# Optimization experiments

Hardware: AMD Instinct MI355X
Metric: run time of the kernel (lower is better)

Reference implementation:

```python
import jax, jax.numpy as jnp
import numpy as np

B, T, I, H = 256, 512, 3, 32  # batch, seq_len, input_size, hidden_size


def setup_inputs() -> dict:
    key = jax.random.key(0)
    ks = jax.random.split(key, 24)
    bound = 1.0 / np.sqrt(H)  # PyTorch LSTM init: U(-1/sqrt(H), 1/sqrt(H))

    def u(k, shape):
        return jax.random.uniform(k, shape, jnp.float32, -bound, bound)

    inp = {"x": jax.random.normal(ks[0], (B, T, I), jnp.float32)}
    idx = 1
    for l, insz in [(0, I), (1, 2 * H)]:
        for d in "fb":
            inp[f"w_ih_l{l}{d}"] = u(ks[idx], (4 * H, insz)); idx += 1
            inp[f"w_hh_l{l}{d}"] = u(ks[idx], (4 * H, H)); idx += 1
            inp[f"b_ih_l{l}{d}"] = u(ks[idx], (4 * H,)); idx += 1
            inp[f"b_hh_l{l}{d}"] = u(ks[idx], (4 * H,)); idx += 1
    inp["wc1"] = u(ks[idx], (32, 2 * H)); idx += 1
    inp["bc1"] = u(ks[idx], (32,)); idx += 1
    inp["wc2"] = u(ks[idx], (2, 32)); idx += 1
    inp["bc2"] = u(ks[idx], (2,))
    return inp


def _lstm_dir(x, w_ih, w_hh, b_ih, b_hh, reverse):
    """One direction of one LSTM layer. x: [B,T,in]. Returns (hs [B,T,H], h_final [B,H])."""
    Bb, Hh = x.shape[0], w_hh.shape[1]
    # precompute input contribution for all timesteps: [T,B,4H]
    gx = jnp.einsum('bti,gi->tbg', x, w_ih) + (b_ih + b_hh)

    def step(carry, g):
        h, c = carry
        z = g + h @ w_hh.T  # [B,4H], gate order i,f,g,o (PyTorch)
        i, f, gg, o = jnp.split(z, 4, axis=-1)
        c = jax.nn.sigmoid(f) * c + jax.nn.sigmoid(i) * jnp.tanh(gg)
        h = jax.nn.sigmoid(o) * jnp.tanh(c)
        return (h, c), h

    init = (jnp.zeros((Bb, Hh), x.dtype), jnp.zeros((Bb, Hh), x.dtype))
    (h_final, _), hs = jax.lax.scan(step, init, gx, reverse=reverse)
    return jnp.swapaxes(hs, 0, 1), h_final


def reference(x,
              w_ih_l0f, w_hh_l0f, b_ih_l0f, b_hh_l0f,
              w_ih_l0b, w_hh_l0b, b_ih_l0b, b_hh_l0b,
              w_ih_l1f, w_hh_l1f, b_ih_l1f, b_hh_l1f,
              w_ih_l1b, w_hh_l1b, b_ih_l1b, b_hh_l1b,
              wc1, bc1, wc2, bc2):
    # Layer 0, both directions (dropout between layers disabled: eval mode)
    hs0f, _ = _lstm_dir(x, w_ih_l0f, w_hh_l0f, b_ih_l0f, b_hh_l0f, False)
    hs0b, _ = _lstm_dir(x, w_ih_l0b, w_hh_l0b, b_ih_l0b, b_hh_l0b, True)
    h0 = jnp.concatenate([hs0f, hs0b], axis=-1)  # [B,T,2H]
    # Layer 1: only final hidden states needed
    _, h1f = _lstm_dir(h0, w_ih_l1f, w_hh_l1f, b_ih_l1f, b_hh_l1f, False)
    _, h1b = _lstm_dir(h0, w_ih_l1b, w_hh_l1b, b_ih_l1b, b_hh_l1b, True)
    hn = jnp.concatenate([h1f, h1b], axis=-1)  # [B,2H] == torch.cat([hn[-2], hn[-1]], 1)
    # Classifier head (Dropout is identity in eval)
    hidden = jax.nn.relu(hn @ wc1.T + bc1)
    return hidden @ wc2.T + bc2  # [B,2] logits
```

## Files before the change

### kernel.cpp

```cpp
#include <hip/hip_runtime.h>
#include <cstdint>

#define T_SEQ 512
#define BATCH 256
#define HID   32

__device__ __forceinline__ float rcp_fast(float x) {
    return __builtin_amdgcn_rcpf(x);
}
__device__ __forceinline__ float sigf(float x) {
    return rcp_fast(1.0f + __expf(-x));
}
__device__ __forceinline__ float tanhf_fast(float x) {
    return fmaf(2.0f, rcp_fast(1.0f + __expf(-2.0f * x)), -1.0f);
}
__device__ __forceinline__ float rdlane(float v, int lane) {
    return __uint_as_float(__builtin_amdgcn_readlane(__float_as_uint(v), lane));
}

#if defined(__has_builtin)
#  if __has_builtin(__builtin_amdgcn_permlane32_swap)
#    define HAVE_PLSWAP 1
#  endif
#endif
#ifndef HAVE_PLSWAP
#  define HAVE_PLSWAP 0
#endif

__device__ __forceinline__ float swap_half(float z) {
#if HAVE_PLSWAP
    typedef int int2v __attribute__((ext_vector_type(2)));
    unsigned zu = __float_as_uint(z);
    int2v r = __builtin_amdgcn_permlane32_swap((int)zu, (int)zu, false, false);
    return __uint_as_float((unsigned)r.x ^ (unsigned)r.y ^ zu);
#else
    return __shfl_xor(z, 32);
#endif
}

#define LD4(p) (*(const float4*)(p))

#define WGRP(NM, PTR, OFF)                                                   \
    float NM##0, NM##1, NM##2, NM##3;                                        \
    { float4 _t = LD4((PTR) + (OFF)); NM##0 = _t.x; NM##1 = _t.y;            \
      NM##2 = _t.z; NM##3 = _t.w; }

#define KEEP4(NM)                                                            \
    asm volatile("" : "+v"(NM##0), "+v"(NM##1), "+v"(NM##2), "+v"(NM##3));

#define WLOAD_ALL(whh_)                                                      \
    WGRP(wa0_, whh_, ra*HID+ 0) WGRP(wa1_, whh_, ra*HID+ 4)                  \
    WGRP(wa2_, whh_, ra*HID+ 8) WGRP(wa3_, whh_, ra*HID+12)                  \
    WGRP(wa4_, whh_, ra*HID+16) WGRP(wa5_, whh_, ra*HID+20)                  \
    WGRP(wa6_, whh_, ra*HID+24) WGRP(wa7_, whh_, ra*HID+28)                  \
    WGRP(wb0_, whh_, rb*HID+ 0) WGRP(wb1_, whh_, rb*HID+ 4)                  \
    WGRP(wb2_, whh_, rb*HID+ 8) WGRP(wb3_, whh_, rb*HID+12)                  \
    WGRP(wb4_, whh_, rb*HID+16) WGRP(wb5_, whh_, rb*HID+20)                  \
    WGRP(wb6_, whh_, rb*HID+24) WGRP(wb7_, whh_, rb*HID+28)

#define KEEPW                                                                \
    KEEP4(wa0_) KEEP4(wa1_) KEEP4(wa2_) KEEP4(wa3_)                          \
    KEEP4(wa4_) KEEP4(wa5_) KEEP4(wa6_) KEEP4(wa7_)                          \
    KEEP4(wb0_) KEEP4(wb1_) KEEP4(wb2_) KEEP4(wb3_)                          \
    KEEP4(wb4_) KEEP4(wb5_) KEEP4(wb6_) KEEP4(wb7_)

#define HF(NMA, NMB, k)                                                      \
    a0 = fmaf(NMA##0, hs[(k)+0], a0); a1 = fmaf(NMA##1, hs[(k)+1], a1);      \
    a2 = fmaf(NMA##2, hs[(k)+2], a2); a3 = fmaf(NMA##3, hs[(k)+3], a3);      \
    c0 = fmaf(NMB##0, hs[(k)+0], c0); c1 = fmaf(NMB##1, hs[(k)+1], c1);      \
    c2 = fmaf(NMB##2, hs[(k)+2], c2); c3 = fmaf(NMB##3, hs[(k)+3], c3);

#define HFMA_ALL                                                             \
    HF(wa0_, wb0_,  0) HF(wa1_, wb1_,  4) HF(wa2_, wb2_,  8)                 \
    HF(wa3_, wb3_, 12) HF(wa4_, wb4_, 16) HF(wa5_, wb5_, 20)                 \
    HF(wa6_, wb6_, 24) HF(wa7_, wb7_, 28)

__global__ void __launch_bounds__(64)
__attribute__((amdgpu_waves_per_eu(1, 1)))
lstm_l0(const float* __restrict__ x,
        const float* __restrict__ wih_f, const float* __restrict__ whh_f,
        const float* __restrict__ bih_f, const float* __restrict__ bhh_f,
        const float* __restrict__ wih_b, const float* __restrict__ whh_b,
        const float* __restrict__ bih_b, const float* __restrict__ bhh_b,
        float* __restrict__ h0)
{
    const int l   = threadIdx.x;
    const int u   = l & 31;
    const int hi  = l >> 5;
    const int bid = blockIdx.x;
    const int dir = bid >> 8;
    const int b   = bid & 255;

    const float* wih = dir ? wih_b : wih_f;
    const float* whh = dir ? whh_b : whh_f;
    const float* bih = dir ? bih_b : bih_f;
    const float* bhh = dir ? bhh_b : bhh_f;

    const int ra = l;
    const int rb = 64 + l;

    WLOAD_ALL(whh)

    float wia0 = wih[ra*3+0], wia1 = wih[ra*3+1], wia2 = wih[ra*3+2];
    float wib0 = wih[rb*3+0], wib1 = wih[rb*3+1], wib2 = wih[rb*3+2];
    float basa = bih[ra] + bhh[ra];
    float basb = bih[rb] + bhh[rb];

    float hs[HID];
#pragma unroll
    for (int k = 0; k < HID; ++k) hs[k] = 0.0f;
    float c = 0.0f;

    const float* xb   = x  + (size_t)b * T_SEQ * 3;
    float*       outp = h0 + (size_t)b * T_SEQ * 64 + dir * HID + u;

    int t = dir ? (T_SEQ - 1) : 0;
    const int step = dir ? -1 : 1;

    float x0 = xb[t*3+0], x1 = xb[t*3+1], x2 = xb[t*3+2];
    float xga = fmaf(wia2, x2, fmaf(wia1, x1, fmaf(wia0, x0, basa)));
    float xgb = fmaf(wib2, x2, fmaf(wib1, x1, fmaf(wib0, x0, basb)));
    {
        int tn = t + step;
        x0 = xb[tn*3+0]; x1 = xb[tn*3+1]; x2 = xb[tn*3+2];
    }

    for (int s = 0; s < T_SEQ; ++s) {
        KEEPW
        asm volatile("" : "+v"(wia0), "+v"(wia1), "+v"(wia2), "+v"(basa));
        asm volatile("" : "+v"(wib0), "+v"(wib1), "+v"(wib2), "+v"(basb));

        float xgaN = fmaf(wia2, x2, fmaf(wia1, x1, fmaf(wia0, x0, basa)));
        float xgbN = fmaf(wib2, x2, fmaf(wib1, x1, fmaf(wib0, x0, basb)));
        {
            int sn = (s + 2 < T_SEQ) ? (s + 2) : (T_SEQ - 1);
            int tn = dir ? (T_SEQ - 1 - sn) : sn;
            x0 = xb[tn*3+0]; x1 = xb[tn*3+1]; x2 = xb[tn*3+2];
        }

        float a0 = xga, a1 = 0.f, a2 = 0.f, a3 = 0.f;
        float c0 = xgb, c1 = 0.f, c2 = 0.f, c3 = 0.f;
        HFMA_ALL
        float za = (a0 + a1) + (a2 + a3);
        float zb = (c0 + c1) + (c2 + c3);

        float fa = swap_half(za);
        float fb = swap_half(zb);
        float zi = hi ? fa : za;
        float zf = hi ? za : fa;
        float zg = hi ? fb : zb;
        float zo = hi ? zb : fb;

        c = sigf(zf) * c + sigf(zi) * tanhf_fast(zg);
        float h = sigf(zo) * tanhf_fast(c);

        if (hi == 0) outp[(size_t)t * 64] = h;

#pragma unroll
        for (int k = 0; k < HID; ++k) hs[k] = rdlane(h, k);

        xga = xgaN; xgb = xgbN;
        t += step;
    }
}

#define WRLOAD_ALL(w_)                                                       \
    WGRP(wr0_,  w_, j*64+ 0) WGRP(wr1_,  w_, j*64+ 4)                        \
    WGRP(wr2_,  w_, j*64+ 8) WGRP(wr3_,  w_, j*64+12)                        \
    WGRP(wr4_,  w_, j*64+16) WGRP(wr5_,  w_, j*64+20)                        \
    WGRP(wr6_,  w_, j*64+24) WGRP(wr7_,  w_, j*64+28)                        \
    WGRP(wr8_,  w_, j*64+32) WGRP(wr9_,  w_, j*64+36)                        \
    WGRP(wr10_, w_, j*64+40) WGRP(wr11_, w_, j*64+44)                        \
    WGRP(wr12_, w_, j*64+48) WGRP(wr13_, w_, j*64+52)                        \
    WGRP(wr14_, w_, j*64+56) WGRP(wr15_, w_, j*64+60)

#define KEEPWR                                                               \
    KEEP4(wr0_)  KEEP4(wr1_)  KEEP4(wr2_)  KEEP4(wr3_)                       \
    KEEP4(wr4_)  KEEP4(wr5_)  KEEP4(wr6_)  KEEP4(wr7_)                       \
    KEEP4(wr8_)  KEEP4(wr9_)  KEEP4(wr10_) KEEP4(wr11_)                      \
    KEEP4(wr12_) KEEP4(wr13_) KEEP4(wr14_) KEEP4(wr15_)

#define GF1(ARR, q, NM)                                                      \
    a0 = fmaf(ARR[q].x, NM##0, a0); a1 = fmaf(ARR[q].y, NM##1, a1);          \
    a2 = fmaf(ARR[q].z, NM##2, a2); a3 = fmaf(ARR[q].w, NM##3, a3);

#define GFALL(ARR)                                                           \
    GF1(ARR, 0, wr0_)  GF1(ARR, 1, wr1_)  GF1(ARR, 2, wr2_)                  \
    GF1(ARR, 3, wr3_)  GF1(ARR, 4, wr4_)  GF1(ARR, 5, wr5_)                  \
    GF1(ARR, 6, wr6_)  GF1(ARR, 7, wr7_)  GF1(ARR, 8, wr8_)                  \
    GF1(ARR, 9, wr9_)  GF1(ARR,10, wr10_) GF1(ARR,11, wr11_)                 \
    GF1(ARR,12, wr12_) GF1(ARR,13, wr13_) GF1(ARR,14, wr14_)                 \
    GF1(ARR,15, wr15_)

__global__ void __launch_bounds__(256)
__attribute__((amdgpu_waves_per_eu(2, 2)))
gx1_gemm(const float* __restrict__ h0,
         const float* __restrict__ w_f, const float* __restrict__ bi_f, const float* __restrict__ bh_f,
         const float* __restrict__ w_b, const float* __restrict__ bi_b, const float* __restrict__ bh_b,
         float* __restrict__ gxo)
{
    const int tid = threadIdx.x;
    const int d = tid >> 7, j = tid & 127;
    const int t = blockIdx.x;

    const float* w = d ? w_b : w_f;
    WRLOAD_ALL(w)
    const float bias = d ? (bi_b[j] + bh_b[j]) : (bi_f[j] + bh_f[j]);

    float* outp = gxo + ((size_t)d * T_SEQ + t) * ((size_t)BATCH * 128) + j;
    const float* base = h0 + (size_t)t * 64;

    float4 A[16], B4[16];
#pragma unroll
    for (int q = 0; q < 16; ++q) A[q] = LD4(base + q*4);

    for (int b = 0; b < BATCH; b += 2) {
        KEEPWR
        {
            const float* p = base + (size_t)(b + 1) * (T_SEQ * 64);
#pragma unroll
            for (int q = 0; q < 16; ++q) B4[q] = LD4(p + q*4);
        }
        {
            float a0 = bias, a1 = 0.f, a2 = 0.f, a3 = 0.f;
            GFALL(A)
            outp[(size_t)b * 128] = (a0 + a1) + (a2 + a3);
        }
        if (b + 2 < BATCH) {
            const float* p = base + (size_t)(b + 2) * (T_SEQ * 64);
#pragma unroll
            for (int q = 0; q < 16; ++q) A[q] = LD4(p + q*4);
        }
        {
            float a0 = bias, a1 = 0.f, a2 = 0.f, a3 = 0.f;
            GFALL(B4)
            outp[(size_t)(b + 1) * 128] = (a0 + a1) + (a2 + a3);
        }
    }
}

__global__ void __launch_bounds__(64)
__attribute__((amdgpu_waves_per_eu(1, 1)))
lstm_l1(const float* __restrict__ gx,
        const float* __restrict__ whh_f, const float* __restrict__ whh_b,
        float* __restrict__ hn)
{
    const int l   = threadIdx.x;
    const int u   = l & 31;
    const int hi  = l >> 5;
    const int bid = blockIdx.x;
    const int dir = bid >> 8;
    const int b   = bid & 255;

    const float* whh = dir ? whh_b : whh_f;
    const int ra = l, rb = 64 + l;

    WLOAD_ALL(whh)

    float hs[HID];
#pragma unroll
    for (int k = 0; k < HID; ++k) hs[k] = 0.0f;
    float c = 0.0f;

    const size_t TS = (size_t)BATCH * 128;
    const float* gp = gx + ((size_t)dir * T_SEQ * BATCH + b) * 128;

    int t = dir ? (T_SEQ - 1) : 0;
    const int step = dir ? -1 : 1;

    float ga0 = gp[(size_t)t * TS + ra];
    float gb0 = gp[(size_t)t * TS + rb];
    float ga1, gb1;
    {
        int t1 = t + step;
        ga1 = gp[(size_t)t1 * TS + ra];
        gb1 = gp[(size_t)t1 * TS + rb];
    }

    float h = 0.0f;
    for (int s = 0; s < T_SEQ; ++s) {
        KEEPW

        float gaN, gbN;
        {
            int sn = (s + 2 < T_SEQ) ? (s + 2) : (T_SEQ - 1);
            int tn = dir ? (T_SEQ - 1 - sn) : sn;
            gaN = gp[(size_t)tn * TS + ra];
            gbN = gp[(size_t)tn * TS + rb];
        }

        float a0 = ga0, a1 = 0.f, a2 = 0.f, a3 = 0.f;
        float c0 = gb0, c1 = 0.f, c2 = 0.f, c3 = 0.f;
        HFMA_ALL
        float za = (a0 + a1) + (a2 + a3);
        float zb = (c0 + c1) + (c2 + c3);

        float fa = swap_half(za);
        float fb = swap_half(zb);
        float zi = hi ? fa : za;
        float zf = hi ? za : fa;
        float zg = hi ? fb : zb;
        float zo = hi ? zb : fb;

        c = sigf(zf) * c + sigf(zi) * tanhf_fast(zg);
        h = sigf(zo) * tanhf_fast(c);

#pragma unroll
        for (int k = 0; k < HID; ++k) hs[k] = rdlane(h, k);

        ga0 = ga1; gb0 = gb1; ga1 = gaN; gb1 = gbN;
        t += step;
    }
    if (hi == 0) hn[(size_t)b * 64 + dir * HID + u] = h;
}

__global__ void __launch_bounds__(64)
classifier(const float* __restrict__ hn,
           const float* __restrict__ wc1,
           const float* __restrict__ bc1,
           const float* __restrict__ wc2,
           const float* __restrict__ bc2,
           float* __restrict__ out)
{
    const int b = blockIdx.x, tid = threadIdx.x;
    __shared__ float hsm[64];
    __shared__ float hidden[32];
    hsm[tid] = hn[(size_t)b * 64 + tid];
    __syncthreads();
    if (tid < 32) {
        float a = bc1[tid];
#pragma unroll
        for (int k = 0; k < 64; ++k) a = fmaf(wc1[tid*64 + k], hsm[k], a);
        hidden[tid] = fmaxf(a, 0.0f);
    }
    __syncthreads();
    if (tid < 2) {
        float a = bc2[tid];
#pragma unroll
        for (int k = 0; k < 32; ++k) a = fmaf(wc2[tid*32 + k], hidden[k], a);
        out[(size_t)b * 2 + tid] = a;
    }
}

extern "C" void kernel_launch(void* const* d_in, const int* in_sizes, int n_in,
                              void* d_out, int out_size, void* d_ws, size_t ws_size,
                              hipStream_t stream) {
    const float* x        = (const float*)d_in[0];
    const float* w_ih_l0f = (const float*)d_in[1];
    const float* w_hh_l0f = (const float*)d_in[2];
    const float* b_ih_l0f = (const float*)d_in[3];
    const float* b_hh_l0f = (const float*)d_in[4];
    const float* w_ih_l0b = (const float*)d_in[5];
    const float* w_hh_l0b = (const float*)d_in[6];
    const float* b_ih_l0b = (const float*)d_in[7];
    const float* b_hh_l0b = (const float*)d_in[8];
    const float* w_ih_l1f = (const float*)d_in[9];
    const float* w_hh_l1f = (const float*)d_in[10];
    const float* b_ih_l1f = (const float*)d_in[11];
    const float* b_hh_l1f = (const float*)d_in[12];
    const float* w_ih_l1b = (const float*)d_in[13];
    const float* w_hh_l1b = (const float*)d_in[14];
    const float* b_ih_l1b = (const float*)d_in[15];
    const float* b_hh_l1b = (const float*)d_in[16];
    const float* wc1      = (const float*)d_in[17];
    const float* bc1      = (const float*)d_in[18];
    const float* wc2      = (const float*)d_in[19];
    const float* bc2      = (const float*)d_in[20];
    float* out = (float*)d_out;

    char* ws = (char*)d_ws;
    float* h0  = (float*)(ws);
    float* gx1 = (float*)(ws + 33554432);
    float* hn  = (float*)(ws + 33554432 + 134217728);

    lstm_l0<<<dim3(512), dim3(64), 0, stream>>>(
        x, w_ih_l0f, w_hh_l0f, b_ih_l0f, b_hh_l0f,
           w_ih_l0b, w_hh_l0b, b_ih_l0b, b_hh_l0b, h0);

    gx1_gemm<<<dim3(T_SEQ), dim3(256), 0, stream>>>(
        h0, w_ih_l1f, b_ih_l1f, b_hh_l1f,
            w_ih_l1b, b_ih_l1b, b_hh_l1b, gx1);

    lstm_l1<<<dim3(512), dim3(64), 0, stream>>>(
        gx1, w_hh_l1f, w_hh_l1b, hn);

    classifier<<<dim3(BATCH), dim3(64), 0, stream>>>(
        hn, wc1, bc1, wc2, bc2, out);
}
```

Before: 681.6 us.

## Process two batch sequences per wavefront in both LSTM recurrence kernels

```diff
diff --git a/kernel.cpp b/kernel.cpp
--- a/kernel.cpp
+++ b/kernel.cpp
@@ -64,16 +64,32 @@
     KEEP4(wb0_) KEEP4(wb1_) KEEP4(wb2_) KEEP4(wb3_)                          \
     KEEP4(wb4_) KEEP4(wb5_) KEEP4(wb6_) KEEP4(wb7_)
 
-#define HF(NMA, NMB, k)                                                      \
-    a0 = fmaf(NMA##0, hs[(k)+0], a0); a1 = fmaf(NMA##1, hs[(k)+1], a1);      \
-    a2 = fmaf(NMA##2, hs[(k)+2], a2); a3 = fmaf(NMA##3, hs[(k)+3], a3);      \
-    c0 = fmaf(NMB##0, hs[(k)+0], c0); c1 = fmaf(NMB##1, hs[(k)+1], c1);      \
-    c2 = fmaf(NMB##2, hs[(k)+2], c2); c3 = fmaf(NMB##3, hs[(k)+3], c3);
-
-#define HFMA_ALL                                                             \
-    HF(wa0_, wb0_,  0) HF(wa1_, wb1_,  4) HF(wa2_, wb2_,  8)                 \
-    HF(wa3_, wb3_, 12) HF(wa4_, wb4_, 16) HF(wa5_, wb5_, 20)                 \
-    HF(wa6_, wb6_, 24) HF(wa7_, wb7_, 28)
+#define HF2(NMA, NMB, k)                                                     \
+    aA0 = fmaf(NMA##0, hsA[(k)+0], aA0); aA1 = fmaf(NMA##1, hsA[(k)+1], aA1);\
+    aA2 = fmaf(NMA##2, hsA[(k)+2], aA2); aA3 = fmaf(NMA##3, hsA[(k)+3], aA3);\
+    cA0 = fmaf(NMB##0, hsA[(k)+0], cA0); cA1 = fmaf(NMB##1, hsA[(k)+1], cA1);\
+    cA2 = fmaf(NMB##2, hsA[(k)+2], cA2); cA3 = fmaf(NMB##3, hsA[(k)+3], cA3);\
+    aB0 = fmaf(NMA##0, hsB[(k)+0], aB0); aB1 = fmaf(NMA##1, hsB[(k)+1], aB1);\
+    aB2 = fmaf(NMA##2, hsB[(k)+2], aB2); aB3 = fmaf(NMA##3, hsB[(k)+3], aB3);\
+    cB0 = fmaf(NMB##0, hsB[(k)+0], cB0); cB1 = fmaf(NMB##1, hsB[(k)+1], cB1);\
+    cB2 = fmaf(NMB##2, hsB[(k)+2], cB2); cB3 = fmaf(NMB##3, hsB[(k)+3], cB3);
+
+#define HFMA2_ALL                                                            \
+    HF2(wa0_, wb0_,  0) HF2(wa1_, wb1_,  4) HF2(wa2_, wb2_,  8)              \
+    HF2(wa3_, wb3_, 12) HF2(wa4_, wb4_, 16) HF2(wa5_, wb5_, 20)              \
+    HF2(wa6_, wb6_, 24) HF2(wa7_, wb7_, 28)
+
+#define GATES(ZA, ZB, C, H)                                                  \
+    {                                                                        \
+        float fa = swap_half(ZA);                                            \
+        float fb = swap_half(ZB);                                            \
+        float zi = hi ? fa : ZA;                                             \
+        float zf = hi ? ZA : fa;                                             \
+        float zg = hi ? fb : ZB;                                             \
+        float zo = hi ? ZB : fb;                                             \
+        C = sigf(zf) * C + sigf(zi) * tanhf_fast(zg);                        \
+        H = sigf(zo) * tanhf_fast(C);                                        \
+    }
 
 __global__ void __launch_bounds__(64)
 __attribute__((amdgpu_waves_per_eu(1, 1)))
@@ -84,12 +100,14 @@
         const float* __restrict__ bih_b, const float* __restrict__ bhh_b,
         float* __restrict__ h0)
 {
-    const int l   = threadIdx.x;
-    const int u   = l & 31;
-    const int hi  = l >> 5;
-    const int bid = blockIdx.x;
-    const int dir = bid >> 8;
-    const int b   = bid & 255;
+    const int l    = threadIdx.x;
+    const int u    = l & 31;
+    const int hi   = l >> 5;
+    const int bid  = blockIdx.x;
+    const int dir  = bid >> 7;
+    const int pair = bid & 127;
+    const int b0   = pair * 2;
+    const int b1   = b0 + 1;
 
     const float* wih = dir ? wih_b : wih_f;
     const float* whh = dir ? whh_b : whh_f;
@@ -106,23 +124,29 @@
     float basa = bih[ra] + bhh[ra];
     float basb = bih[rb] + bhh[rb];
 
-    float hs[HID];
-#pragma unroll
-    for (int k = 0; k < HID; ++k) hs[k] = 0.0f;
-    float c = 0.0f;
-
-    const float* xb   = x  + (size_t)b * T_SEQ * 3;
-    float*       outp = h0 + (size_t)b * T_SEQ * 64 + dir * HID + u;
+    float hsA[HID], hsB[HID];
+#pragma unroll
+    for (int k = 0; k < HID; ++k) { hsA[k] = 0.0f; hsB[k] = 0.0f; }
+    float cA = 0.0f, cB = 0.0f;
+
+    const float* xbA  = x  + (size_t)b0 * T_SEQ * 3;
+    const float* xbB  = x  + (size_t)b1 * T_SEQ * 3;
+    float*       outA = h0 + (size_t)b0 * T_SEQ * 64 + dir * HID + u;
+    float*       outB = h0 + (size_t)b1 * T_SEQ * 64 + dir * HID + u;
 
     int t = dir ? (T_SEQ - 1) : 0;
     const int step = dir ? -1 : 1;
 
-    float x0 = xb[t*3+0], x1 = xb[t*3+1], x2 = xb[t*3+2];
-    float xga = fmaf(wia2, x2, fmaf(wia1, x1, fmaf(wia0, x0, basa)));
-    float xgb = fmaf(wib2, x2, fmaf(wib1, x1, fmaf(wib0, x0, basb)));
+    float xA0 = xbA[t*3+0], xA1 = xbA[t*3+1], xA2 = xbA[t*3+2];
+    float xB0 = xbB[t*3+0], xB1 = xbB[t*3+1], xB2 = xbB[t*3+2];
+    float xgaA = fmaf(wia2, xA2, fmaf(wia1, xA1, fmaf(wia0, xA0, basa)));
+    float xgbA = fmaf(wib2, xA2, fmaf(wib1, xA1, fmaf(wib0, xA0, basb)));
+    float xgaB = fmaf(wia2, xB2, fmaf(wia1, xB1, fmaf(wia0, xB0, basa)));
+    float xgbB = fmaf(wib2, xB2, fmaf(wib1, xB1, fmaf(wib0, xB0, basb)));
     {
         int tn = t + step;
-        x0 = xb[tn*3+0]; x1 = xb[tn*3+1]; x2 = xb[tn*3+2];
+        xA0 = xbA[tn*3+0]; xA1 = xbA[tn*3+1]; xA2 = xbA[tn*3+2];
+        xB0 = xbB[tn*3+0]; xB1 = xbB[tn*3+1]; xB2 = xbB[tn*3+2];
     }
 
     for (int s = 0; s < T_SEQ; ++s) {
@@ -130,36 +154,42 @@
         asm volatile("" : "+v"(wia0), "+v"(wia1), "+v"(wia2), "+v"(basa));
         asm volatile("" : "+v"(wib0), "+v"(wib1), "+v"(wib2), "+v"(basb));
 
-        float xgaN = fmaf(wia2, x2, fmaf(wia1, x1, fmaf(wia0, x0, basa)));
-        float xgbN = fmaf(wib2, x2, fmaf(wib1, x1, fmaf(wib0, x0, basb)));
+        float xgaAN = fmaf(wia2, xA2, fmaf(wia1, xA1, fmaf(wia0, xA0, basa)));
+        float xgbAN = fmaf(wib2, xA2, fmaf(wib1, xA1, fmaf(wib0, xA0, basb)));
+        float xgaBN = fmaf(wia2, xB2, fmaf(wia1, xB1, fmaf(wia0, xB0, basa)));
+        float xgbBN = fmaf(wib2, xB2, fmaf(wib1, xB1, fmaf(wib0, xB0, basb)));
         {
             int sn = (s + 2 < T_SEQ) ? (s + 2) : (T_SEQ - 1);
             int tn = dir ? (T_SEQ - 1 - sn) : sn;
-            x0 = xb[tn*3+0]; x1 = xb[tn*3+1]; x2 = xb[tn*3+2];
-        }
-
-        float a0 = xga, a1 = 0.f, a2 = 0.f, a3 = 0.f;
-        float c0 = xgb, c1 = 0.f, c2 = 0.f, c3 = 0.f;
-        HFMA_ALL
-        float za = (a0 + a1) + (a2 + a3);
-        float zb = (c0 + c1) + (c2 + c3);
-
-        float fa = swap_half(za);
-        float fb = swap_half(zb);
-        float zi = hi ? fa : za;
-        float zf = hi ? za : fa;
-        float zg = hi ? fb : zb;
-        float zo = hi ? zb : fb;
-
-        c = sigf(zf) * c + sigf(zi) * tanhf_fast(zg);
-        float h = sigf(zo) * tanhf_fast(c);
-
-        if (hi == 0) outp[(size_t)t * 64] = h;
-
-#pragma unroll
-        for (int k = 0; k < HID; ++k) hs[k] = rdlane(h, k);
-
-        xga = xgaN; xgb = xgbN;
+            xA0 = xbA[tn*3+0]; xA1 = xbA[tn*3+1]; xA2 = xbA[tn*3+2];
+            xB0 = xbB[tn*3+0]; xB1 = xbB[tn*3+1]; xB2 = xbB[tn*3+2];
+        }
+
+        float aA0 = xgaA, aA1 = 0.f, aA2 = 0.f, aA3 = 0.f;
+        float cA0 = xgbA, cA1 = 0.f, cA2 = 0.f, cA3 = 0.f;
+        float aB0 = xgaB, aB1 = 0.f, aB2 = 0.f, aB3 = 0.f;
+        float cB0 = xgbB, cB1 = 0.f, cB2 = 0.f, cB3 = 0.f;
+        HFMA2_ALL
+        float zaA = (aA0 + aA1) + (aA2 + aA3);
+        float zbA = (cA0 + cA1) + (cA2 + cA3);
+        float zaB = (aB0 + aB1) + (aB2 + aB3);
+        float zbB = (cB0 + cB1) + (cB2 + cB3);
+
+        float hA, hB;
+        GATES(zaA, zbA, cA, hA)
+        GATES(zaB, zbB, cB, hB)
+
+        if (hi == 0) {
+            outA[(size_t)t * 64] = hA;
+            outB[(size_t)t * 64] = hB;
+        }
+
+#pragma unroll
+        for (int k = 0; k < HID; ++k) hsA[k] = rdlane(hA, k);
+#pragma unroll
+        for (int k = 0; k < HID; ++k) hsB[k] = rdlane(hB, k);
+
+        xgaA = xgaAN; xgbA = xgbAN; xgaB = xgaBN; xgbB = xgbBN;
         t += step;
     }
 }
@@ -245,73 +275,79 @@
         const float* __restrict__ whh_f, const float* __restrict__ whh_b,
         float* __restrict__ hn)
 {
-    const int l   = threadIdx.x;
-    const int u   = l & 31;
-    const int hi  = l >> 5;
-    const int bid = blockIdx.x;
-    const int dir = bid >> 8;
-    const int b   = bid & 255;
+    const int l    = threadIdx.x;
+    const int u    = l & 31;
+    const int hi   = l >> 5;
+    const int bid  = blockIdx.x;
+    const int dir  = bid >> 7;
+    const int pair = bid & 127;
+    const int b0   = pair * 2;
+    const int b1   = b0 + 1;
 
     const float* whh = dir ? whh_b : whh_f;
     const int ra = l, rb = 64 + l;
 
     WLOAD_ALL(whh)
 
-    float hs[HID];
-#pragma unroll
-    for (int k = 0; k < HID; ++k) hs[k] = 0.0f;
-    float c = 0.0f;
+    float hsA[HID], hsB[HID];
+#pragma unroll
+    for (int k = 0; k < HID; ++k) { hsA[k] = 0.0f; hsB[k] = 0.0f; }
+    float cA = 0.0f, cB = 0.0f;
 
     const size_t TS = (size_t)BATCH * 128;
-    const float* gp = gx + ((size_t)dir * T_SEQ * BATCH + b) * 128;
+    const float* gpA = gx + ((size_t)dir * T_SEQ * BATCH + b0) * 128;
+    const float* gpB = gx + ((size_t)dir * T_SEQ * BATCH + b1) * 128;
 
     int t = dir ? (T_SEQ - 1) : 0;
     const int step = dir ? -1 : 1;
 
-    float ga0 = gp[(size_t)t * TS + ra];
-    float gb0 = gp[(size_t)t * TS + rb];
-    float ga1, gb1;
+    float gaA0 = gpA[(size_t)t * TS + ra], gbA0 = gpA[(size_t)t * TS + rb];
+    float gaB0 = gpB[(size_t)t * TS + ra], gbB0 = gpB[(size_t)t * TS + rb];
+    float gaA1, gbA1, gaB1, gbB1;
     {
         int t1 = t + step;
-        ga1 = gp[(size_t)t1 * TS + ra];
-        gb1 = gp[(size_t)t1 * TS + rb];
-    }
-
-    float h = 0.0f;
+        gaA1 = gpA[(size_t)t1 * TS + ra]; gbA1 = gpA[(size_t)t1 * TS + rb];
+        gaB1 = gpB[(size_t)t1 * TS + ra]; gbB1 = gpB[(size_t)t1 * TS + rb];
+    }
+
+    float hA = 0.0f, hB = 0.0f;
     for (int s = 0; s < T_SEQ; ++s) {
         KEEPW
 
-        float gaN, gbN;
+        float gaAN, gbAN, gaBN, gbBN;
         {
             int sn = (s + 2 < T_SEQ) ? (s + 2) : (T_SEQ - 1);
             int tn = dir ? (T_SEQ - 1 - sn) : sn;
-            gaN = gp[(size_t)tn * TS + ra];
-            gbN = gp[(size_t)tn * TS + rb];
-        }
-
-        float a0 = ga0, a1 = 0.f, a2 = 0.f, a3 = 0.f;
-        float c0 = gb0, c1 = 0.f, c2 = 0.f, c3 = 0.f;
-        HFMA_ALL
-        float za = (a0 + a1) + (a2 + a3);
-        float zb = (c0 + c1) + (c2 + c3);
-
-        float fa = swap_half(za);
-        float fb = swap_half(zb);
-        float zi = hi ? fa : za;
-        float zf = hi ? za : fa;
-        float zg = hi ? fb : zb;
-        float zo = hi ? zb : fb;
-
-        c = sigf(zf) * c + sigf(zi) * tanhf_fast(zg);
-        h = sigf(zo) * tanhf_fast(c);
-
-#pragma unroll
-        for (int k = 0; k < HID; ++k) hs[k] = rdlane(h, k);
-
-        ga0 = ga1; gb0 = gb1; ga1 = gaN; gb1 = gbN;
+            gaAN = gpA[(size_t)tn * TS + ra]; gbAN = gpA[(size_t)tn * TS + rb];
+            gaBN = gpB[(size_t)tn * TS + ra]; gbBN = gpB[(size_t)tn * TS + rb];
+        }
+
+        float aA0 = gaA0, aA1 = 0.f, aA2 = 0.f, aA3 = 0.f;
+        float cA0 = gbA0, cA1 = 0.f, cA2 = 0.f, cA3 = 0.f;
+        float aB0 = gaB0, aB1 = 0.f, aB2 = 0.f, aB3 = 0.f;
+        float cB0 = gbB0, cB1 = 0.f, cB2 = 0.f, cB3 = 0.f;
+        HFMA2_ALL
+        float zaA = (aA0 + aA1) + (aA2 + aA3);
+        float zbA = (cA0 + cA1) + (cA2 + cA3);
+        float zaB = (aB0 + aB1) + (aB2 + aB3);
+        float zbB = (cB0 + cB1) + (cB2 + cB3);
+
+        GATES(zaA, zbA, cA, hA)
+        GATES(zaB, zbB, cB, hB)
+
+#pragma unroll
+        for (int k = 0; k < HID; ++k) hsA[k] = rdlane(hA, k);
+#pragma unroll
+        for (int k = 0; k < HID; ++k) hsB[k] = rdlane(hB, k);
+
+        gaA0 = gaA1; gbA0 = gbA1; gaA1 = gaAN; gbA1 = gbAN;
+        gaB0 = gaB1; gbB0 = gbB1; gaB1 = gaBN; gbB1 = gbBN;
         t += step;
     }
-    if (hi == 0) hn[(size_t)b * 64 + dir * HID + u] = h;
+    if (hi == 0) {
+        hn[(size_t)b0 * 64 + dir * HID + u] = hA;
+        hn[(size_t)b1 * 64 + dir * HID + u] = hB;
+    }
 }
 
 __global__ void __launch_bounds__(64)
@@ -373,7 +409,7 @@
     float* gx1 = (float*)(ws + 33554432);
     float* hn  = (float*)(ws + 33554432 + 134217728);
 
-    lstm_l0<<<dim3(512), dim3(64), 0, stream>>>(
+    lstm_l0<<<dim3(256), dim3(64), 0, stream>>>(
         x, w_ih_l0f, w_hh_l0f, b_ih_l0f, b_hh_l0f,
            w_ih_l0b, w_hh_l0b, b_ih_l0b, b_hh_l0b, h0);
 
@@ -381,7 +417,7 @@
         h0, w_ih_l1f, b_ih_l1f, b_hh_l1f,
             w_ih_l1b, b_ih_l1b, b_hh_l1b, gx1);
 
-    lstm_l1<<<dim3(512), dim3(64), 0, stream>>>(
+    lstm_l1<<<dim3(256), dim3(64), 0, stream>>>(
         gx1, w_hh_l1f, w_hh_l1b, hn);
 
     classifier<<<dim3(BATCH), dim3(64), 0, stream>>>(
```

After: 923.8 us. +35.5%, slower.
